# Performance work log

Hardware: AMD Instinct MI355X
Metric: run time of the kernel (lower is better)

The kernel has to match this reference:

```python
import jax, jax.numpy as jnp
import numpy as np

H, D, H1, L = 4, 128, 512, 2
EPS = 1e-5


def _seg_softmax(logits, seg, n):
    # numerically stable softmax over edges grouped by destination node
    mx = jax.ops.segment_max(logits, seg, num_segments=n)
    mx = jnp.where(jnp.isfinite(mx), mx, 0.0)
    e = jnp.exp(logits - mx[seg])
    s = jax.ops.segment_sum(e, seg, num_segments=n)
    return e / (s[seg] + 1e-16)


def _layernorm(x, g, b):
    mu = x.mean(-1, keepdims=True)
    var = ((x - mu) ** 2).mean(-1, keepdims=True)
    return (x - mu) * jax.lax.rsqrt(var + EPS) * g + b


def _hgt_forward(x_paper, x_author, Wp_paper, bp_paper, Wp_author, bp_author,
                 Wk, bk, Wq, bq, Wv, bv, Wa, ba, skip,
                 a_rel, m_rel, p_rel, ln_g, ln_b,
                 W256, b256, W128, b128,
                 ei_cites, ei_writes, ei_writtenby):
    Np, Na = x_paper.shape[0], x_author.shape[0]
    hp = x_paper @ Wp_paper + bp_paper   # [Np, 512]
    ha = x_author @ Wp_author + bp_author  # [Na, 512]
    scale = 1.0 / jnp.sqrt(jnp.float32(D))

    def kqv(h, l, t):
        k = (h @ Wk[l, t] + bk[l, t]).reshape(-1, H, D)
        q = (h @ Wq[l, t] + bq[l, t]).reshape(-1, H, D)
        v = (h @ Wv[l, t] + bv[l, t]).reshape(-1, H, D)
        return k, q, v

    def rel_msgs(k_src, v_src, q_dst, ei, l, r):
        src, dst = ei[0], ei[1]
        kr = jnp.einsum('nhd,hde->nhe', k_src, a_rel[l, r])  # per-src-node relation transform
        vr = jnp.einsum('nhd,hde->nhe', v_src, m_rel[l, r])
        alpha = (q_dst[dst] * kr[src]).sum(-1) * p_rel[l, r] * scale  # [E, H]
        return alpha, vr[src], dst

    for l in range(L):
        kp, qp, vp = kqv(hp, l, 0)
        ka, qa, va = kqv(ha, l, 1)
        # paper receives: cites (paper->paper, rel 0) + writes (author->paper, rel 1)
        a0, m0, d0 = rel_msgs(kp, vp, qp, ei_cites, l, 0)
        a1, m1, d1 = rel_msgs(ka, va, qp, ei_writes, l, 1)
        al = jnp.concatenate([a0, a1], 0)
        mg = jnp.concatenate([m0, m1], 0)
        ds = jnp.concatenate([d0, d1], 0)
        al = _seg_softmax(al, ds, Np)
        op = jax.ops.segment_sum(al[:, :, None] * mg, ds, num_segments=Np).reshape(Np, H1)
        # author receives: written_by (paper->author, rel 2)
        a2, m2, d2 = rel_msgs(kp, vp, qa, ei_writtenby, l, 2)
        a2 = _seg_softmax(a2, d2, Na)
        oa = jax.ops.segment_sum(a2[:, :, None] * m2, d2, num_segments=Na).reshape(Na, H1)
        # per-dst-type output linear on gelu, then sigmoid-gated skip (HGTConv)
        op = jax.nn.gelu(op, approximate=False) @ Wa[l, 0] + ba[l, 0]
        oa = jax.nn.gelu(oa, approximate=False) @ Wa[l, 1] + ba[l, 1]
        sp = jax.nn.sigmoid(skip[l, 0])
        sa = jax.nn.sigmoid(skip[l, 1])
        op = sp * op + (1.0 - sp) * hp
        oa = sa * oa + (1.0 - sa) * ha
        # encoder wrapper: residual + shared LayerNorm + ReLU (dropout = identity in eval)
        hp = jax.nn.relu(_layernorm(op + hp, ln_g[l], ln_b[l]))
        ha = jax.nn.relu(_layernorm(oa + ha, ln_g[l], ln_b[l]))

    hp = jax.nn.relu(hp @ W256 + b256) @ W128 + b128
    ha = jax.nn.relu(ha @ W256 + b256) @ W128 + b128
    return hp, ha


def setup_inputs() -> dict:
    key = jax.random.key(0)
    ks = iter(jax.random.split(key, 48))
    Np, Na, IN = 30000, 10000, 768
    Ec, Ew, Eb = 150000, 80000, 80000
    f = lambda *s: jax.random.normal(next(ks), s, jnp.float32) * 0.02
    ri = lambda n, e: jax.random.randint(next(ks), (e,), 0, n, jnp.int32)
    inp = {
        'x_paper': jax.random.normal(next(ks), (Np, IN), jnp.float32),
        'x_author': jax.random.normal(next(ks), (Na, IN), jnp.float32),
        'Wp_paper': f(IN, H1), 'bp_paper': jnp.zeros((H1,), jnp.float32),
        'Wp_author': f(IN, H1), 'bp_author': jnp.zeros((H1,), jnp.float32),
        'Wk': f(L, 2, H1, H1), 'bk': jnp.zeros((L, 2, H1), jnp.float32),
        'Wq': f(L, 2, H1, H1), 'bq': jnp.zeros((L, 2, H1), jnp.float32),
        'Wv': f(L, 2, H1, H1), 'bv': jnp.zeros((L, 2, H1), jnp.float32),
        'Wa': f(L, 2, H1, H1), 'ba': jnp.zeros((L, 2, H1), jnp.float32),
        'skip': jnp.ones((L, 2), jnp.float32),
        'a_rel': f(L, 3, H, D, D), 'm_rel': f(L, 3, H, D, D),
        'p_rel': jnp.ones((L, 3, H), jnp.float32),
        'ln_g': jnp.ones((L, H1), jnp.float32), 'ln_b': jnp.zeros((L, H1), jnp.float32),
        'W256': f(H1, 256), 'b256': jnp.zeros((256,), jnp.float32),
        'W128': f(256, 128), 'b128': jnp.zeros((128,), jnp.float32),
        'ei_cites': jnp.stack([ri(Np, Ec), ri(Np, Ec)]),
        'ei_writes': jnp.stack([ri(Na, Ew), ri(Np, Ew)]),
        'ei_writtenby': jnp.stack([ri(Np, Eb), ri(Na, Eb)]),
    }
    return inp


def reference(x_paper, x_author, Wp_paper, bp_paper, Wp_author, bp_author,
              Wk, bk, Wq, bq, Wv, bv, Wa, ba, skip,
              a_rel, m_rel, p_rel, ln_g, ln_b,
              W256, b256, W128, b128,
              ei_cites, ei_writes, ei_writtenby):
    return _hgt_forward(x_paper, x_author, Wp_paper, bp_paper, Wp_author, bp_author,
                        Wk, bk, Wq, bq, Wv, bv, Wa, ba, skip,
                        a_rel, m_rel, p_rel, ln_g, ln_b,
                        W256, b256, W128, b128,
                        ei_cites, ei_writes, ei_writtenby)
```

## Files before the change

kernel.cpp:

```cpp
#include <hip/hip_runtime.h>
#include <hip/hip_bf16.h>
#include <math.h>

#define NHEAD 4
#define DH 128
#define HID 512
#define NLAY 2
#define NP 30000
#define NA 10000
#define INDIM 768
#define EC 150000
#define EW 80000
#define EB 80000
#define NQP 2560
#define NQA 1536

typedef __hip_bfloat16 bf16;
typedef __attribute__((ext_vector_type(8))) short bf16x8;
typedef __attribute__((ext_vector_type(4))) float f32x4;
typedef __attribute__((ext_vector_type(4))) unsigned int u32x4;

__device__ __forceinline__ unsigned short f2bu(float f){ bf16 t = __float2bfloat16(f); return *(unsigned short*)&t; }
__device__ __forceinline__ float bu2f(unsigned short u){ return __uint_as_float((unsigned)u << 16); }

__device__ __forceinline__ void load8b(const bf16* __restrict__ p, int i8, float* o){
  uint4 r = ((const uint4*)p)[i8];
  o[0]=__uint_as_float(r.x<<16); o[1]=__uint_as_float(r.x&0xffff0000u);
  o[2]=__uint_as_float(r.y<<16); o[3]=__uint_as_float(r.y&0xffff0000u);
  o[4]=__uint_as_float(r.z<<16); o[5]=__uint_as_float(r.z&0xffff0000u);
  o[6]=__uint_as_float(r.w<<16); o[7]=__uint_as_float(r.w&0xffff0000u);
}

__device__ __forceinline__ void gload16(const void* g, void* l) {
  __builtin_amdgcn_global_load_lds((const __attribute__((address_space(1))) void*)g,
                                   (__attribute__((address_space(3))) void*)l, 16, 0, 0);
}

struct GemmPair {
  const bf16 *A0, *A1, *B0, *B1;
  const float *b0, *b1;
  void *C0, *C1;
  int lda0, lda1, ldb0, ldb1, ldc0, ldc1;
  int M0, M1, K0, K1;
  int act0, act1, bf0, bf1;
  int nbn0, nbn1, nw0;
};

#define TSTRIDE 132

__global__ __launch_bounds__(256)
void mfma_gemm2(GemmPair gp)
{
  __shared__ __align__(16) short smem[32768];
  const int tid = threadIdx.x;
  const int lane = tid & 63, w = tid >> 6;
  const int nwg = gridDim.x;
  const int bid = blockIdx.x;
  const int xcd = bid & 7, pos = bid >> 3;
  const int q8 = nwg >> 3, r8 = nwg & 7;
  const int work = (xcd < r8 ? xcd * (q8 + 1) : r8 * (q8 + 1) + (xcd - r8) * q8) + pos;
  const int g = work >= gp.nw0;
  const int w2 = g ? work - gp.nw0 : work;
  const bf16* A  = g ? gp.A1 : gp.A0;
  const bf16* Bt = g ? gp.B1 : gp.B0;
  const float* bias = g ? gp.b1 : gp.b0;
  void* Cv = g ? gp.C1 : gp.C0;
  const int lda = g ? gp.lda1 : gp.lda0;
  const int ldb = g ? gp.ldb1 : gp.ldb0;
  const int ldc = g ? gp.ldc1 : gp.ldc0;
  const int M = g ? gp.M1 : gp.M0;
  const int K = g ? gp.K1 : gp.K0;
  const int act = g ? gp.act1 : gp.act0;
  const int isbf = g ? gp.bf1 : gp.bf0;
  const int nbn = g ? gp.nbn1 : gp.nbn0;
  const int brow = (w2 / nbn) * 128, bcol = (w2 % nbn) * 128;
  const int wr = w >> 1, wc = w & 1;

  f32x4 acc[4][4];
#pragma unroll
  for (int m = 0; m < 4; m++)
#pragma unroll
    for (int n = 0; n < 4; n++) acc[m][n] = (f32x4){0.f, 0.f, 0.f, 0.f};

  auto STAGE = [&](int buf, int k0) {
    short* Asb = smem + buf * 8192;
    short* Bsb = smem + 16384 + buf * 8192;
#pragma unroll
    for (int i = 0; i < 4; i++) {
      int chunk = i * 4 + w;
      int c_lin = chunk * 64 + lane;
      int row = c_lin >> 3;
      int kc = ((c_lin & 7) ^ (row & 7)) * 8;
      int growA = brow + row; growA = growA < M ? growA : M - 1;
      gload16(A + (size_t)growA * lda + k0 + kc, Asb + chunk * 512);
      gload16(Bt + (size_t)(bcol + row) * ldb + k0 + kc, Bsb + chunk * 512);
    }
  };

  const int nk = K >> 6;
  STAGE(0, 0);
  __syncthreads();
  int buf = 0;
  for (int t = 0; t < nk; t++) {
    if (t + 1 < nk) STAGE(buf ^ 1, (t + 1) << 6);
    const short* Asb = smem + buf * 8192;
    const short* Bsb = smem + 16384 + buf * 8192;
#pragma unroll
    for (int kk = 0; kk < 2; kk++) {
      const int ke = kk * 32 + (lane >> 4) * 8;
      bf16x8 af[4], bq[4];
#pragma unroll
      for (int m = 0; m < 4; m++) {
        int row = wr * 64 + m * 16 + (lane & 15);
        af[m] = *(const bf16x8*)(Asb + row * 64 + (ke ^ ((row & 7) << 3)));
      }
#pragma unroll
      for (int n = 0; n < 4; n++) {
        int col = wc * 64 + n * 16 + (lane & 15);
        bq[n] = *(const bf16x8*)(Bsb + col * 64 + (ke ^ ((col & 7) << 3)));
      }
#pragma unroll
      for (int m = 0; m < 4; m++)
#pragma unroll
        for (int n = 0; n < 4; n++)
          acc[m][n] = __builtin_amdgcn_mfma_f32_16x16x32_bf16(af[m], bq[n], acc[m][n], 0, 0, 0);
    }
    __syncthreads();
    buf ^= 1;
  }

  if (isbf) {
#pragma unroll
    for (int m = 0; m < 4; m++) {
      int row0 = wr * 64 + m * 16 + (lane >> 4) * 4;
#pragma unroll
      for (int n = 0; n < 4; n++) {
        int col = wc * 64 + n * 16 + (lane & 15);
        float bv = bias ? bias[bcol + col] : 0.f;
#pragma unroll
        for (int r = 0; r < 4; r++) {
          float v = acc[m][n][r] + bv;
          if (act) v = fmaxf(v, 0.f);
          smem[(row0 + r) * TSTRIDE + col] = (short)f2bu(v);
        }
      }
    }
    __syncthreads();
#pragma unroll
    for (int it = 0; it < 8; it++) {
      int chunk = it * 256 + tid;
      int row = chunk >> 4, c16 = chunk & 15;
      int gr = brow + row;
      if (gr < M) {
        u32x4 v = *(const u32x4*)(smem + row * TSTRIDE + c16 * 8);
        __builtin_nontemporal_store(v,
            (u32x4*)((unsigned short*)Cv + (size_t)gr * ldc + bcol + c16 * 8));
      }
    }
  } else {
#pragma unroll
    for (int m = 0; m < 4; m++) {
      int gr0 = brow + wr * 64 + m * 16 + (lane >> 4) * 4;
#pragma unroll
      for (int n = 0; n < 4; n++) {
        int gc = bcol + wc * 64 + n * 16 + (lane & 15);
        float bv = bias ? bias[gc] : 0.f;
#pragma unroll
        for (int r = 0; r < 4; r++) {
          int gr = gr0 + r;
          if (gr < M) {
            float v = acc[m][n][r] + bv;
            if (act) v = fmaxf(v, 0.f);
            __builtin_nontemporal_store(v, (float*)Cv + (size_t)gr * ldc + gc);
          }
        }
      }
    }
  }
}

struct FuseArgs {
  const float* W[12];
  const float* rel[12];
  const float* bin[12];
  float* out[12];
  float* bout[12];
};
struct TrArgs {
  const float* src[20];
  bf16* dst[20];
};
struct CopyB { const float* src[4]; float* dst[4]; };

__global__ __launch_bounds__(256)
void gemm_fuse(FuseArgs fa)
{
  int c = blockIdx.z >> 2, h = blockIdx.z & 3;
  const float* A = fa.W[c] + h * 128;
  const float* B = fa.rel[c] + (size_t)h * 128 * 128;
  float* C = fa.out[c] + h * 128;
  __shared__ float Ast[64][17];
  __shared__ float Bst[16][64];
  const int tid = threadIdx.x;
  const int tx = tid & 15, ty = tid >> 4;
  const int bm = blockIdx.x * 64, bn = blockIdx.y * 64;
  float acc[4][4] = {};
  for (int k0 = 0; k0 < 128; k0 += 16) {
#pragma unroll
    for (int i = 0; i < 4; i++) {
      int lin = tid + i * 256;
      int m = lin >> 4, kk = lin & 15;
      Ast[m][kk] = A[(size_t)(bm + m) * 512 + k0 + kk];
      int kb = lin >> 6, nb = lin & 63;
      Bst[kb][nb] = B[(size_t)(k0 + kb) * 128 + bn + nb];
    }
    __syncthreads();
#pragma unroll
    for (int kk = 0; kk < 16; kk++) {
      float a[4], b[4];
#pragma unroll
      for (int i = 0; i < 4; i++) a[i] = Ast[ty * 4 + i][kk];
#pragma unroll
      for (int j = 0; j < 4; j++) b[j] = Bst[kk][tx * 4 + j];
#pragma unroll
      for (int i = 0; i < 4; i++)
#pragma unroll
        for (int j = 0; j < 4; j++)
          acc[i][j] = fmaf(a[i], b[j], acc[i][j]);
    }
    __syncthreads();
  }
#pragma unroll
  for (int i = 0; i < 4; i++)
#pragma unroll
    for (int j = 0; j < 4; j++)
      C[(size_t)(bm + ty * 4 + i) * 512 + bn + tx * 4 + j] = acc[i][j];
}

__global__ __launch_bounds__(256)
void transpose20(TrArgs ta)
{
  int c = blockIdx.z;
  const float* in = ta.src[c];
  bf16* o = ta.dst[c];
  __shared__ float t[32][33];
  int bn = blockIdx.x * 32, bk = blockIdx.y * 32;
  int x = threadIdx.x, y = threadIdx.y;
#pragma unroll
  for (int i = 0; i < 32; i += 8)
    t[y + i][x] = in[(size_t)(bk + y + i) * 512 + bn + x];
  __syncthreads();
#pragma unroll
  for (int i = 0; i < 32; i += 8)
    o[(size_t)(bn + y + i) * 512 + bk + x] = __float2bfloat16(t[x][y + i]);
}

__global__ __launch_bounds__(512)
void bias_fuse_all(FuseArgs fa)
{
  int c = blockIdx.x;
  int j = threadIdx.x;
  int h = j >> 7, e = j & 127;
  const float* bh = fa.bin[c] + h * DH;
  const float* rh = fa.rel[c] + (size_t)h * DH * DH;
  float s = 0.f;
  for (int d = 0; d < DH; d++) s = fmaf(bh[d], rh[d * DH + e], s);
  fa.bout[c][j] = s;
}

__global__ __launch_bounds__(512)
void copy_bias(CopyB cb)
{
  cb.dst[blockIdx.x][threadIdx.x] = cb.src[blockIdx.x][threadIdx.x];
}

__global__ __launch_bounds__(256)
void transpose_to_bf16(const float* __restrict__ in, bf16* __restrict__ out,
                       int K_, int N_)
{
  __shared__ float t[32][33];
  int bn = blockIdx.x * 32, bk = blockIdx.y * 32;
  int x = threadIdx.x, y = threadIdx.y;
#pragma unroll
  for (int i = 0; i < 32; i += 8) {
    int k = bk + y + i, n = bn + x;
    if (k < K_ && n < N_) t[y + i][x] = in[(size_t)k * N_ + n];
  }
  __syncthreads();
#pragma unroll
  for (int i = 0; i < 32; i += 8) {
    int n = bn + y + i, k = bk + x;
    if (n < N_ && k < K_) out[(size_t)n * K_ + k] = __float2bfloat16(t[x][y + i]);
  }
}

__global__ __launch_bounds__(256)
void f32_to_bf16_2(const float* __restrict__ s0, bf16* __restrict__ d0, long long n0,
                   const float* __restrict__ s1, bf16* __restrict__ d1, long long n1)
{
  long long i = ((long long)blockIdx.x * 256 + threadIdx.x) * 4;
  const float* s; bf16* d;
  if (i < n0) { s = s0; d = d0; }
  else { i -= n0; if (i >= n1) return; s = s1; d = d1; }
  float4 v = *(const float4*)(s + i);
  ushort4 o;
  o.x = f2bu(v.x); o.y = f2bu(v.y); o.z = f2bu(v.z); o.w = f2bu(v.w);
  *(ushort4*)(d + i) = o;
}

__global__ __launch_bounds__(256)
void build_hist(const int* __restrict__ ei_dst, int E, int* __restrict__ deg)
{
  int i = blockIdx.x * 256 + threadIdx.x;
  if (i < E) atomicAdd(&deg[ei_dst[i]], 1);
}

__global__ __launch_bounds__(256)
void scan_blk(const int* __restrict__ deg, int n, int* __restrict__ rowptr,
              int* __restrict__ bsum)
{
  __shared__ int sh[256];
  int t = threadIdx.x;
  int base = blockIdx.x * 1024 + t * 4;
  int v0 = 0, v1 = 0, v2 = 0, v3 = 0;
  if (base + 3 < n) {
    int4 v = *(const int4*)(deg + base);
    v0 = v.x; v1 = v.y; v2 = v.z; v3 = v.w;
  } else {
    if (base < n)     v0 = deg[base];
    if (base + 1 < n) v1 = deg[base + 1];
    if (base + 2 < n) v2 = deg[base + 2];
    if (base + 3 < n) v3 = deg[base + 3];
  }
  int s = v0 + v1 + v2 + v3;
  sh[t] = s;
  __syncthreads();
#pragma unroll
  for (int off = 1; off < 256; off <<= 1) {
    int tv = (t >= off) ? sh[t - off] : 0;
    __syncthreads();
    sh[t] += tv;
    __syncthreads();
  }
  int excl = sh[t] - s;
  if (t == 255) bsum[blockIdx.x] = sh[255];
  if (base < n)     rowptr[base] = excl;
  if (base + 1 < n) rowptr[base + 1] = excl + v0;
  if (base + 2 < n) rowptr[base + 2] = excl + v0 + v1;
  if (base + 3 < n) rowptr[base + 3] = excl + v0 + v1 + v2;
}

__global__ __launch_bounds__(64)
void scan_bsum(int* __restrict__ bsum, int nb, int* __restrict__ rowptr_end)
{
  int t = threadIdx.x;
  int v = (t < nb) ? bsum[t] : 0;
  int inc = v;
#pragma unroll
  for (int off = 1; off < 64; off <<= 1) {
    int o = __shfl_up(inc, off);
    if (t >= off) inc += o;
  }
  if (t < nb) bsum[t] = inc - v;
  if (t == nb - 1) *rowptr_end = inc;
}

__global__ __launch_bounds__(256)
void scan_add(int* __restrict__ rowptr, const int* __restrict__ bsum, int n)
{
  int add = bsum[blockIdx.x];
  if (add == 0) return;
  int i = blockIdx.x * 1024 + threadIdx.x * 4;
  if (i < n)     rowptr[i] += add;
  if (i + 1 < n) rowptr[i + 1] += add;
  if (i + 2 < n) rowptr[i + 2] += add;
  if (i + 3 < n) rowptr[i + 3] += add;
}

__global__ __launch_bounds__(256)
void build_scatter(const int* __restrict__ ei, int E, int flag,
                   const int* __restrict__ rowptr, int* __restrict__ cursor,
                   int* __restrict__ srcs)
{
  int e = blockIdx.x * 256 + threadIdx.x;
  if (e >= E) return;
  int src = ei[e];
  int dst = ei[E + e];
  int pos = rowptr[dst] + atomicAdd(&cursor[dst], 1);
  srcs[pos] = src | flag;
}

__global__ __launch_bounds__(256)
void csr_attn_agg2(const int* __restrict__ rowptrP, const int* __restrict__ srcsP,
                   const int* __restrict__ rowptrA, const int* __restrict__ srcsA,
                   const bf16* __restrict__ qkvP, const bf16* __restrict__ qkvA,
                   const float* __restrict__ prl, float scale,
                   bf16* __restrict__ agP, bf16* __restrict__ agA)
{
  int node = blockIdx.x * 4 + (threadIdx.x >> 6);
  int lane = threadIdx.x & 63;
  int h = lane >> 4;
  const int* rp; const int* srcs;
  const bf16* q; const bf16 *t0, *t1;
  int ld0, off0, ld1, off1;
  float p0, p1;
  bf16* outp;
  if (node < NP) {
    rp = rowptrP; srcs = srcsP;
    q = qkvP + (size_t)node * NQP;
    t0 = qkvP; ld0 = NQP; off0 = 512;
    t1 = qkvA; ld1 = NQA; off1 = 512;
    p0 = prl[h] * scale; p1 = prl[4 + h] * scale;
    outp = agP + (size_t)node * HID;
  } else {
    int r = node - NP;
    if (r >= NA) return;
    rp = rowptrA; srcs = srcsA; node = r;
    q = qkvA + (size_t)r * NQA;
    t0 = qkvP; ld0 = NQP; off0 = 1536;
    t1 = qkvP; ld1 = NQP; off1 = 1536;
    p0 = prl[8 + h] * scale; p1 = p0;
    outp = agA + (size_t)r * HID;
  }
  float qv[8];
  load8b(q, lane, qv);
  int beg = rp[node], end = rp[node + 1];
  float m = -INFINITY, s = 0.f;
  float acc[8] = {};
  for (int p = beg; p < end; ++p) {
    int se = srcs[p];
    int src = se & 0x3FFFFFFF;
    bool f1 = (se & 0x40000000) != 0;
    const bf16* row = f1 ? (t1 + (size_t)src * ld1 + off1)
                         : (t0 + (size_t)src * ld0 + off0);
    float kv[8], vv[8];
    load8b(row, lane, kv);
    load8b(row + 512, lane, vv);
    float a = 0.f;
#pragma unroll
    for (int i = 0; i < 8; i++) a = fmaf(qv[i], kv[i], a);
    a += __shfl_xor(a, 1);
    a += __shfl_xor(a, 2);
    a += __shfl_xor(a, 4);
    a += __shfl_xor(a, 8);
    a *= f1 ? p1 : p0;
    if (a > m + 8.f) {
      float sc = __expf(m - a);
      s *= sc;
#pragma unroll
      for (int i = 0; i < 8; i++) acc[i] *= sc;
      m = a;
    }
    float wgt = __expf(a - m);
    s += wgt;
#pragma unroll
    for (int i = 0; i < 8; i++) acc[i] = fmaf(wgt, vv[i], acc[i]);
  }
  float inv = 1.f / (s + 1e-16f);
  unsigned short gg[8];
#pragma unroll
  for (int i = 0; i < 8; i++) {
    float v = acc[i] * inv;
    gg[i] = f2bu(0.5f * v * (1.f + erff(v * 0.70710678118654752f)));
  }
  uint4 o;
  o.x = gg[0] | ((unsigned)gg[1] << 16);
  o.y = gg[2] | ((unsigned)gg[3] << 16);
  o.z = gg[4] | ((unsigned)gg[5] << 16);
  o.w = gg[6] | ((unsigned)gg[7] << 16);
  *(uint4*)(outp + lane * 8) = o;
}

__global__ __launch_bounds__(256)
void skip_ln_relu2(const bf16* __restrict__ oplP, const bf16* __restrict__ oplA,
                   bf16* __restrict__ hP, bf16* __restrict__ hA,
                   const float* __restrict__ skip2,
                   const float* __restrict__ g, const float* __restrict__ b)
{
  int row = blockIdx.x;
  const bf16* orow; bf16* hrow; float sk;
  if (row < NP) {
    orow = oplP + (size_t)row * HID; hrow = hP + (size_t)row * HID; sk = skip2[0];
  } else {
    int r = row - NP;
    orow = oplA + (size_t)r * HID; hrow = hA + (size_t)r * HID; sk = skip2[1];
  }
  float sp = 1.f / (1.f + expf(-sk));
  int t = threadIdx.x;
  ushort2 ov = ((const ushort2*)orow)[t];
  ushort2 hv = ((ushort2*)hrow)[t];
  float t0 = sp * bu2f(ov.x) + (2.f - sp) * bu2f(hv.x);
  float t1 = sp * bu2f(ov.y) + (2.f - sp) * bu2f(hv.y);
  float s = t0 + t1, ss = t0 * t0 + t1 * t1;
#pragma unroll
  for (int off = 32; off; off >>= 1) {
    s += __shfl_down(s, off);
    ss += __shfl_down(ss, off);
  }
  __shared__ float sh[8];
  int wid = t >> 6, lane = t & 63;
  if (lane == 0) { sh[wid] = s; sh[4 + wid] = ss; }
  __syncthreads();
  if (t == 0) {
    float S = 0, SS = 0;
    for (int wv = 0; wv < 4; wv++) { S += sh[wv]; SS += sh[4 + wv]; }
    sh[0] = S; sh[4] = SS;
  }
  __syncthreads();
  float mu = sh[0] * (1.f / 512.f);
  float var = sh[4] * (1.f / 512.f) - mu * mu;
  float inv = rsqrtf(var + 1e-5f);
  float y0 = (t0 - mu) * inv * g[2 * t] + b[2 * t];
  float y1 = (t1 - mu) * inv * g[2 * t + 1] + b[2 * t + 1];
  ushort2 o;
  o.x = f2bu(fmaxf(y0, 0.f));
  o.y = f2bu(fmaxf(y1, 0.f));
  ((ushort2*)hrow)[t] = o;
}

static inline void mgemm2(GemmPair gp, int N0, int N1, hipStream_t s)
{
  gp.nbn0 = N0 / 128;
  gp.nbn1 = N1 / 128;
  int nw0 = ((gp.M0 + 127) / 128) * gp.nbn0;
  int nw1 = ((gp.M1 + 127) / 128) * gp.nbn1;
  gp.nw0 = nw0;
  mfma_gemm2<<<dim3(nw0 + nw1), 256, 0, s>>>(gp);
}

extern "C" void kernel_launch(void* const* d_in, const int* in_sizes, int n_in,
                              void* d_out, int out_size, void* d_ws, size_t ws_size,
                              hipStream_t stream)
{
  const float* x_paper  = (const float*)d_in[0];
  const float* x_author = (const float*)d_in[1];
  const float* Wp_paper = (const float*)d_in[2];
  const float* bp_paper = (const float*)d_in[3];
  const float* Wp_author= (const float*)d_in[4];
  const float* bp_author= (const float*)d_in[5];
  const float* Wk = (const float*)d_in[6];
  const float* bk = (const float*)d_in[7];
  const float* Wq = (const float*)d_in[8];
  const float* bq = (const float*)d_in[9];
  const float* Wv = (const float*)d_in[10];
  const float* bv = (const float*)d_in[11];
  const float* Wa = (const float*)d_in[12];
  const float* ba = (const float*)d_in[13];
  const float* skip = (const float*)d_in[14];
  const float* a_rel = (const float*)d_in[15];
  const float* m_rel = (const float*)d_in[16];
  const float* p_rel = (const float*)d_in[17];
  const float* ln_g = (const float*)d_in[18];
  const float* ln_b = (const float*)d_in[19];
  const float* W256 = (const float*)d_in[20];
  const float* b256 = (const float*)d_in[21];
  const float* W128 = (const float*)d_in[22];
  const float* b128 = (const float*)d_in[23];
  const int* ei_c = (const int*)d_in[24];
  const int* ei_w = (const int*)d_in[25];
  const int* ei_b = (const int*)d_in[26];
  float* out = (float*)d_out;

  const size_t NPe = (size_t)NP * HID, NAe = (size_t)NA * HID;
  const size_t HH = (size_t)HID * HID;
  char* w = (char*)d_ws;
  size_t off = 0;
  auto alloc = [&](size_t bytes) -> void* {
    void* p = (void*)(w + off);
    off += (bytes + 255) & ~(size_t)255;
    return p;
  };
  bf16* hb_p  = (bf16*)alloc(NPe * 2);
  bf16* hb_a  = (bf16*)alloc(NAe * 2);
  bf16* qkv_p = (bf16*)alloc((size_t)NP * NQP * 2);
  bf16* qkv_a = (bf16*)alloc((size_t)NA * NQA * 2);
  bf16* ag_p  = (bf16*)alloc(NPe * 2);
  bf16* ag_a  = (bf16*)alloc(NAe * 2);
  float* Wf32 = (float*)alloc(12 * HH * 4);
  bf16* WBtP  = (bf16*)alloc((size_t)2 * NQP * HID * 2);
  bf16* WBtA  = (bf16*)alloc((size_t)2 * NQA * HID * 2);
  float* pbP  = (float*)alloc((size_t)2 * NQP * 4);
  float* pbA  = (float*)alloc((size_t)2 * NQA * 4);
  bf16* WaT   = (bf16*)alloc(4 * HH * 2);
  bf16* W256T = (bf16*)alloc((size_t)HID * 256 * 2);
  bf16* W128T = (bf16*)alloc((size_t)256 * 128 * 2);
  bf16* WpTp  = (bf16*)alloc((size_t)INDIM * HID * 2);
  bf16* WpTa  = (bf16*)alloc((size_t)INDIM * HID * 2);
  int* rowptrP = (int*)alloc((size_t)(NP + 1) * 4);
  int* degP    = (int*)alloc((size_t)NP * 4);
  int* srcsP   = (int*)alloc((size_t)(EC + EW) * 4);
  int* rowptrA = (int*)alloc((size_t)(NA + 1) * 4);
  int* degA    = (int*)alloc((size_t)NA * 4);
  int* srcsA   = (int*)alloc((size_t)EB * 4);
  int* bsumP   = (int*)alloc(64 * 4);
  int* bsumA   = (int*)alloc(64 * 4);
  if (off > ws_size) return;

  const float scale = 0.08838834764831845f;
  const int nbP = (NP + 1023) / 1024, nbA = (NA + 1023) / 1024;

  (void)hipMemsetAsync(degP, 0, (size_t)NP * 4, stream);
  (void)hipMemsetAsync(degA, 0, (size_t)NA * 4, stream);
  build_hist<<<dim3((EC + 255) / 256), 256, 0, stream>>>(ei_c + EC, EC, degP);
  build_hist<<<dim3((EW + 255) / 256), 256, 0, stream>>>(ei_w + EW, EW, degP);
  build_hist<<<dim3((EB + 255) / 256), 256, 0, stream>>>(ei_b + EB, EB, degA);
  scan_blk<<<dim3(nbP), 256, 0, stream>>>(degP, NP, rowptrP, bsumP);
  scan_bsum<<<dim3(1), 64, 0, stream>>>(bsumP, nbP, rowptrP + NP);
  scan_add<<<dim3(nbP), 256, 0, stream>>>(rowptrP, bsumP, NP);
  scan_blk<<<dim3(nbA), 256, 0, stream>>>(degA, NA, rowptrA, bsumA);
  scan_bsum<<<dim3(1), 64, 0, stream>>>(bsumA, nbA, rowptrA + NA);
  scan_add<<<dim3(nbA), 256, 0, stream>>>(rowptrA, bsumA, NA);
  (void)hipMemsetAsync(degP, 0, (size_t)NP * 4, stream);
  (void)hipMemsetAsync(degA, 0, (size_t)NA * 4, stream);
  build_scatter<<<dim3((EC + 255) / 256), 256, 0, stream>>>(ei_c, EC, 0,
      rowptrP, degP, srcsP);
  build_scatter<<<dim3((EW + 255) / 256), 256, 0, stream>>>(ei_w, EW, 0x40000000,
      rowptrP, degP, srcsP);
  build_scatter<<<dim3((EB + 255) / 256), 256, 0, stream>>>(ei_b, EB, 0,
      rowptrA, degA, srcsA);

  FuseArgs fa;
  TrArgs ta;
  CopyB cb;
  for (int l = 0; l < NLAY; l++) {
    bf16* packP = WBtP + (size_t)l * NQP * HID;
    bf16* packA = WBtA + (size_t)l * NQA * HID;
    float* pbPl = pbP + (size_t)l * NQP;
    float* pbAl = pbA + (size_t)l * NQA;
    for (int r = 0; r < 3; r++)
      for (int s = 0; s < 2; s++) {
        int c = (l * 3 + r) * 2 + s;
        int t = (r == 1) ? 1 : 0;
        fa.W[c]   = (s == 0 ? Wk : Wv) + (size_t)(l * 2 + t) * HH;
        fa.rel[c] = (s == 0 ? a_rel : m_rel) + (size_t)(l * 3 + r) * NHEAD * DH * DH;
        fa.bin[c] = (s == 0 ? bk : bv) + (size_t)(l * 2 + t) * HID;
        fa.out[c] = Wf32 + (size_t)c * HH;
        ta.src[c] = fa.out[c];
        if (r == 0) {
          ta.dst[c]  = packP + (size_t)(512 + s * 512) * HID;
          fa.bout[c] = pbPl + 512 + s * 512;
        } else if (r == 1) {
          ta.dst[c]  = packA + (size_t)(512 + s * 512) * HID;
          fa.bout[c] = pbAl + 512 + s * 512;
        } else {
          ta.dst[c]  = packP + (size_t)(1536 + s * 512) * HID;
          fa.bout[c] = pbPl + 1536 + s * 512;
        }
      }
    ta.src[12 + l * 2 + 0] = Wq + (size_t)(l * 2 + 0) * HH;
    ta.dst[12 + l * 2 + 0] = packP;
    ta.src[12 + l * 2 + 1] = Wq + (size_t)(l * 2 + 1) * HH;
    ta.dst[12 + l * 2 + 1] = packA;
    ta.src[16 + l * 2 + 0] = Wa + (size_t)(l * 2 + 0) * HH;
    ta.dst[16 + l * 2 + 0] = WaT + (size_t)(l * 2 + 0) * HH;
    ta.src[16 + l * 2 + 1] = Wa + (size_t)(l * 2 + 1) * HH;
    ta.dst[16 + l * 2 + 1] = WaT + (size_t)(l * 2 + 1) * HH;
    cb.src[l * 2 + 0] = bq + (size_t)(l * 2 + 0) * HID;
    cb.dst[l * 2 + 0] = pbPl;
    cb.src[l * 2 + 1] = bq + (size_t)(l * 2 + 1) * HID;
    cb.dst[l * 2 + 1] = pbAl;
  }
  gemm_fuse<<<dim3(8, 2, 48), 256, 0, stream>>>(fa);
  transpose20<<<dim3(16, 16, 20), dim3(32, 8), 0, stream>>>(ta);
  bias_fuse_all<<<dim3(12), 512, 0, stream>>>(fa);
  copy_bias<<<dim3(4), 512, 0, stream>>>(cb);
  {
    dim3 b(32, 8);
    transpose_to_bf16<<<dim3(8, 16), b, 0, stream>>>(W256, W256T, HID, 256);
    transpose_to_bf16<<<dim3(4, 8), b, 0, stream>>>(W128, W128T, 256, 128);
    transpose_to_bf16<<<dim3(16, 24), b, 0, stream>>>(Wp_paper, WpTp, INDIM, HID);
    transpose_to_bf16<<<dim3(16, 24), b, 0, stream>>>(Wp_author, WpTa, INDIM, HID);
  }

  bf16* xb_p = qkv_p;
  bf16* xb_a = qkv_a;
  long long nxp = (long long)NP * INDIM, nxa = (long long)NA * INDIM;
  f32_to_bf16_2<<<dim3((int)(((nxp + nxa) / 4 + 255) / 256)), 256, 0, stream>>>(
      x_paper, xb_p, nxp, x_author, xb_a, nxa);
  {
    GemmPair gp{};
    gp.A0 = xb_p; gp.lda0 = INDIM; gp.B0 = WpTp; gp.ldb0 = INDIM;
    gp.b0 = bp_paper; gp.C0 = hb_p; gp.ldc0 = HID;
    gp.M0 = NP; gp.K0 = INDIM; gp.act0 = 0; gp.bf0 = 1;
    gp.A1 = xb_a; gp.lda1 = INDIM; gp.B1 = WpTa; gp.ldb1 = INDIM;
    gp.b1 = bp_author; gp.C1 = hb_a; gp.ldc1 = HID;
    gp.M1 = NA; gp.K1 = INDIM; gp.act1 = 0; gp.bf1 = 1;
    mgemm2(gp, HID, HID, stream);
  }

  for (int l = 0; l < NLAY; l++) {
    const float* prl = p_rel + (size_t)l * 3 * NHEAD;
    const bf16* packP = WBtP + (size_t)l * NQP * HID;
    const bf16* packA = WBtA + (size_t)l * NQA * HID;
    const float* pbPl = pbP + (size_t)l * NQP;
    const float* pbAl = pbA + (size_t)l * NQA;

    {
      GemmPair gp{};
      gp.A0 = hb_p; gp.lda0 = HID; gp.B0 = packP; gp.ldb0 = HID;
      gp.b0 = pbPl; gp.C0 = qkv_p; gp.ldc0 = NQP;
      gp.M0 = NP; gp.K0 = HID; gp.act0 = 0; gp.bf0 = 1;
      gp.A1 = hb_a; gp.lda1 = HID; gp.B1 = packA; gp.ldb1 = HID;
      gp.b1 = pbAl; gp.C1 = qkv_a; gp.ldc1 = NQA;
      gp.M1 = NA; gp.K1 = HID; gp.act1 = 0; gp.bf1 = 1;
      mgemm2(gp, NQP, NQA, stream);
    }
    csr_attn_agg2<<<dim3((NP + NA + 3) / 4), 256, 0, stream>>>(
        rowptrP, srcsP, rowptrA, srcsA, qkv_p, qkv_a, prl, scale, ag_p, ag_a);
    bf16* opl_p = qkv_p;
    bf16* opl_a = qkv_a;
    {
      GemmPair gp{};
      gp.A0 = ag_p; gp.lda0 = HID; gp.B0 = WaT + (size_t)(l * 2 + 0) * HH; gp.ldb0 = HID;
      gp.b0 = ba + (size_t)(l * 2 + 0) * HID; gp.C0 = opl_p; gp.ldc0 = HID;
      gp.M0 = NP; gp.K0 = HID; gp.act0 = 0; gp.bf0 = 1;
      gp.A1 = ag_a; gp.lda1 = HID; gp.B1 = WaT + (size_t)(l * 2 + 1) * HH; gp.ldb1 = HID;
      gp.b1 = ba + (size_t)(l * 2 + 1) * HID; gp.C1 = opl_a; gp.ldc1 = HID;
      gp.M1 = NA; gp.K1 = HID; gp.act1 = 0; gp.bf1 = 1;
      mgemm2(gp, HID, HID, stream);
    }
    skip_ln_relu2<<<dim3(NP + NA), 256, 0, stream>>>(
        opl_p, opl_a, hb_p, hb_a, skip + l * 2,
        ln_g + (size_t)l * HID, ln_b + (size_t)l * HID);
  }

  bf16* h256_p = ag_p;
  bf16* h256_a = ag_a;
  {
    GemmPair gp{};
    gp.A0 = hb_p; gp.lda0 = HID; gp.B0 = W256T; gp.ldb0 = HID;
    gp.b0 = b256; gp.C0 = h256_p; gp.ldc0 = 256;
    gp.M0 = NP; gp.K0 = HID; gp.act0 = 1; gp.bf0 = 1;
    gp.A1 = hb_a; gp.lda1 = HID; gp.B1 = W256T; gp.ldb1 = HID;
    gp.b1 = b256; gp.C1 = h256_a; gp.ldc1 = 256;
    gp.M1 = NA; gp.K1 = HID; gp.act1 = 1; gp.bf1 = 1;
    mgemm2(gp, 256, 256, stream);
  }
  {
    GemmPair gp{};
    gp.A0 = h256_p; gp.lda0 = 256; gp.B0 = W128T; gp.ldb0 = 256;
    gp.b0 = b128; gp.C0 = out; gp.ldc0 = 128;
    gp.M0 = NP; gp.K0 = 256; gp.act0 = 0; gp.bf0 = 0;
    gp.A1 = h256_a; gp.lda1 = 256; gp.B1 = W128T; gp.ldb1 = 256;
    gp.b1 = b128; gp.C1 = out + (size_t)NP * 128; gp.ldc1 = 128;
    gp.M1 = NA; gp.K1 = 256; gp.act1 = 0; gp.bf1 = 0;
    mgemm2(gp, 128, 128, stream);
  }
}
```

Before: 898.1 us.

## Merge CSR build launches and single-buffer GEMM shared memory

The per-relation histogram, scan and scatter kernels are merged into combined launches covering all three edge sets, with a single memset for degree and cursor arrays. This cuts roughly a dozen launches and memsets down to six. Separately, the GEMM drops its double-buffered LDS pipeline for a single buffer sized for the epilogue transpose, loading and syncing before each k-step. That lowers LDS use and may allow more resident blocks, but global loads no longer overlap MFMA work.

```diff
diff --git a/kernel.cpp b/kernel.cpp
--- a/kernel.cpp
+++ b/kernel.cpp
@@ -51,7 +51,7 @@
 __global__ __launch_bounds__(256)
 void mfma_gemm2(GemmPair gp)
 {
-  __shared__ __align__(16) short smem[32768];
+  __shared__ __align__(16) short smem[128 * TSTRIDE];
   const int tid = threadIdx.x;
   const int lane = tid & 63, w = tid >> 6;
   const int nwg = gridDim.x;
@@ -82,9 +82,11 @@
 #pragma unroll
     for (int n = 0; n < 4; n++) acc[m][n] = (f32x4){0.f, 0.f, 0.f, 0.f};
 
-  auto STAGE = [&](int buf, int k0) {
-    short* Asb = smem + buf * 8192;
-    short* Bsb = smem + 16384 + buf * 8192;
+  short* Asb = smem;
+  short* Bsb = smem + 8192;
+  const int nk = K >> 6;
+  for (int t = 0; t < nk; t++) {
+    const int k0 = t << 6;
 #pragma unroll
     for (int i = 0; i < 4; i++) {
       int chunk = i * 4 + w;
@@ -95,16 +97,7 @@
       gload16(A + (size_t)growA * lda + k0 + kc, Asb + chunk * 512);
       gload16(Bt + (size_t)(bcol + row) * ldb + k0 + kc, Bsb + chunk * 512);
     }
-  };
-
-  const int nk = K >> 6;
-  STAGE(0, 0);
-  __syncthreads();
-  int buf = 0;
-  for (int t = 0; t < nk; t++) {
-    if (t + 1 < nk) STAGE(buf ^ 1, (t + 1) << 6);
-    const short* Asb = smem + buf * 8192;
-    const short* Bsb = smem + 16384 + buf * 8192;
+    __syncthreads();
 #pragma unroll
     for (int kk = 0; kk < 2; kk++) {
       const int ke = kk * 32 + (lane >> 4) * 8;
@@ -126,7 +119,6 @@
           acc[m][n] = __builtin_amdgcn_mfma_f32_16x16x32_bf16(af[m], bq[n], acc[m][n], 0, 0, 0);
     }
     __syncthreads();
-    buf ^= 1;
   }
 
   if (isbf) {
@@ -309,19 +301,23 @@
 }
 
 __global__ __launch_bounds__(256)
-void build_hist(const int* __restrict__ ei_dst, int E, int* __restrict__ deg)
+void build_hist3(const int* __restrict__ eiC, const int* __restrict__ eiW,
+                 const int* __restrict__ eiB,
+                 int* __restrict__ degP, int* __restrict__ degA)
 {
   int i = blockIdx.x * 256 + threadIdx.x;
-  if (i < E) atomicAdd(&deg[ei_dst[i]], 1);
-}
-
-__global__ __launch_bounds__(256)
-void scan_blk(const int* __restrict__ deg, int n, int* __restrict__ rowptr,
-              int* __restrict__ bsum)
+  if (i < EC) atomicAdd(&degP[eiC[EC + i]], 1);
+  else if (i < EC + EW) atomicAdd(&degP[eiW[EW + (i - EC)]], 1);
+  else if (i < EC + EW + EB) atomicAdd(&degA[eiB[EB + (i - EC - EW)]], 1);
+}
+
+__device__ __forceinline__ void scan_blk_body(const int* __restrict__ deg, int n,
+                                              int* __restrict__ rowptr,
+                                              int* __restrict__ bsum, int blk)
 {
   __shared__ int sh[256];
   int t = threadIdx.x;
-  int base = blockIdx.x * 1024 + t * 4;
+  int base = blk * 1024 + t * 4;
   int v0 = 0, v1 = 0, v2 = 0, v3 = 0;
   if (base + 3 < n) {
     int4 v = *(const int4*)(deg + base);
@@ -343,16 +339,31 @@
     __syncthreads();
   }
   int excl = sh[t] - s;
-  if (t == 255) bsum[blockIdx.x] = sh[255];
+  if (t == 255) bsum[blk] = sh[255];
   if (base < n)     rowptr[base] = excl;
   if (base + 1 < n) rowptr[base + 1] = excl + v0;
   if (base + 2 < n) rowptr[base + 2] = excl + v0 + v1;
   if (base + 3 < n) rowptr[base + 3] = excl + v0 + v1 + v2;
 }
 
+#define NBP ((NP + 1023) / 1024)
+#define NBA ((NA + 1023) / 1024)
+
+__global__ __launch_bounds__(256)
+void scan_blk2(const int* __restrict__ degP, int* __restrict__ rowptrP, int* __restrict__ bsumP,
+               const int* __restrict__ degA, int* __restrict__ rowptrA, int* __restrict__ bsumA)
+{
+  if (blockIdx.x < NBP) scan_blk_body(degP, NP, rowptrP, bsumP, blockIdx.x);
+  else                  scan_blk_body(degA, NA, rowptrA, bsumA, blockIdx.x - NBP);
+}
+
 __global__ __launch_bounds__(64)
-void scan_bsum(int* __restrict__ bsum, int nb, int* __restrict__ rowptr_end)
-{
+void scan_bsum2(int* __restrict__ bsumP, int* __restrict__ endP,
+                int* __restrict__ bsumA, int* __restrict__ endA)
+{
+  int* bsum = blockIdx.x ? bsumA : bsumP;
+  int nb = blockIdx.x ? NBA : NBP;
+  int* rpe = blockIdx.x ? endA : endP;
   int t = threadIdx.x;
   int v = (t < nb) ? bsum[t] : 0;
   int inc = v;
@@ -362,15 +373,19 @@
     if (t >= off) inc += o;
   }
   if (t < nb) bsum[t] = inc - v;
-  if (t == nb - 1) *rowptr_end = inc;
-}
-
-__global__ __launch_bounds__(256)
-void scan_add(int* __restrict__ rowptr, const int* __restrict__ bsum, int n)
-{
-  int add = bsum[blockIdx.x];
+  if (t == nb - 1) *rpe = inc;
+}
+
+__global__ __launch_bounds__(256)
+void scan_add2(int* __restrict__ rowptrP, const int* __restrict__ bsumP,
+               int* __restrict__ rowptrA, const int* __restrict__ bsumA)
+{
+  int* rowptr; const int* bsum; int n, blk;
+  if (blockIdx.x < NBP) { rowptr = rowptrP; bsum = bsumP; n = NP; blk = blockIdx.x; }
+  else                  { rowptr = rowptrA; bsum = bsumA; n = NA; blk = blockIdx.x - NBP; }
+  int add = bsum[blk];
   if (add == 0) return;
-  int i = blockIdx.x * 1024 + threadIdx.x * 4;
+  int i = blk * 1024 + threadIdx.x * 4;
   if (i < n)     rowptr[i] += add;
   if (i + 1 < n) rowptr[i + 1] += add;
   if (i + 2 < n) rowptr[i + 2] += add;
@@ -378,16 +393,29 @@
 }
 
 __global__ __launch_bounds__(256)
-void build_scatter(const int* __restrict__ ei, int E, int flag,
-                   const int* __restrict__ rowptr, int* __restrict__ cursor,
-                   int* __restrict__ srcs)
-{
-  int e = blockIdx.x * 256 + threadIdx.x;
-  if (e >= E) return;
-  int src = ei[e];
-  int dst = ei[E + e];
-  int pos = rowptr[dst] + atomicAdd(&cursor[dst], 1);
-  srcs[pos] = src | flag;
+void build_scatter3(const int* __restrict__ eiC, const int* __restrict__ eiW,
+                    const int* __restrict__ eiB,
+                    const int* __restrict__ rowptrP, int* __restrict__ curP,
+                    int* __restrict__ srcsP,
+                    const int* __restrict__ rowptrA, int* __restrict__ curA,
+                    int* __restrict__ srcsA)
+{
+  int i = blockIdx.x * 256 + threadIdx.x;
+  if (i < EC) {
+    int src = eiC[i], dst = eiC[EC + i];
+    int pos = rowptrP[dst] + atomicAdd(&curP[dst], 1);
+    srcsP[pos] = src;
+  } else if (i < EC + EW) {
+    int e = i - EC;
+    int src = eiW[e], dst = eiW[EW + e];
+    int pos = rowptrP[dst] + atomicAdd(&curP[dst], 1);
+    srcsP[pos] = src | 0x40000000;
+  } else if (i < EC + EW + EB) {
+    int e = i - EC - EW;
+    int src = eiB[e], dst = eiB[EB + e];
+    int pos = rowptrA[dst] + atomicAdd(&curA[dst], 1);
+    srcsA[pos] = src;
+  }
 }
 
 __global__ __launch_bounds__(256)
@@ -587,37 +615,26 @@
   bf16* WpTp  = (bf16*)alloc((size_t)INDIM * HID * 2);
   bf16* WpTa  = (bf16*)alloc((size_t)INDIM * HID * 2);
   int* rowptrP = (int*)alloc((size_t)(NP + 1) * 4);
-  int* degP    = (int*)alloc((size_t)NP * 4);
+  int* rowptrA = (int*)alloc((size_t)(NA + 1) * 4);
+  int* degP    = (int*)alloc((size_t)(2 * NP + 2 * NA) * 4);
+  int* degA    = degP + NP;
+  int* curP    = degA + NA;
+  int* curA    = curP + NP;
   int* srcsP   = (int*)alloc((size_t)(EC + EW) * 4);
-  int* rowptrA = (int*)alloc((size_t)(NA + 1) * 4);
-  int* degA    = (int*)alloc((size_t)NA * 4);
   int* srcsA   = (int*)alloc((size_t)EB * 4);
   int* bsumP   = (int*)alloc(64 * 4);
   int* bsumA   = (int*)alloc(64 * 4);
   if (off > ws_size) return;
 
   const float scale = 0.08838834764831845f;
-  const int nbP = (NP + 1023) / 1024, nbA = (NA + 1023) / 1024;
-
-  (void)hipMemsetAsync(degP, 0, (size_t)NP * 4, stream);
-  (void)hipMemsetAsync(degA, 0, (size_t)NA * 4, stream);
-  build_hist<<<dim3((EC + 255) / 256), 256, 0, stream>>>(ei_c + EC, EC, degP);
-  build_hist<<<dim3((EW + 255) / 256), 256, 0, stream>>>(ei_w + EW, EW, degP);
-  build_hist<<<dim3((EB + 255) / 256), 256, 0, stream>>>(ei_b + EB, EB, degA);
-  scan_blk<<<dim3(nbP), 256, 0, stream>>>(degP, NP, rowptrP, bsumP);
-  scan_bsum<<<dim3(1), 64, 0, stream>>>(bsumP, nbP, rowptrP + NP);
-  scan_add<<<dim3(nbP), 256, 0, stream>>>(rowptrP, bsumP, NP);
-  scan_blk<<<dim3(nbA), 256, 0, stream>>>(degA, NA, rowptrA, bsumA);
-  scan_bsum<<<dim3(1), 64, 0, stream>>>(bsumA, nbA, rowptrA + NA);
-  scan_add<<<dim3(nbA), 256, 0, stream>>>(rowptrA, bsumA, NA);
-  (void)hipMemsetAsync(degP, 0, (size_t)NP * 4, stream);
-  (void)hipMemsetAsync(degA, 0, (size_t)NA * 4, stream);
-  build_scatter<<<dim3((EC + 255) / 256), 256, 0, stream>>>(ei_c, EC, 0,
-      rowptrP, degP, srcsP);
-  build_scatter<<<dim3((EW + 255) / 256), 256, 0, stream>>>(ei_w, EW, 0x40000000,
-      rowptrP, degP, srcsP);
-  build_scatter<<<dim3((EB + 255) / 256), 256, 0, stream>>>(ei_b, EB, 0,
-      rowptrA, degA, srcsA);
+
+  (void)hipMemsetAsync(degP, 0, (size_t)(2 * NP + 2 * NA) * 4, stream);
+  build_hist3<<<dim3((EC + EW + EB + 255) / 256), 256, 0, stream>>>(ei_c, ei_w, ei_b, degP, degA);
+  scan_blk2<<<dim3(NBP + NBA), 256, 0, stream>>>(degP, rowptrP, bsumP, degA, rowptrA, bsumA);
+  scan_bsum2<<<dim3(2), 64, 0, stream>>>(bsumP, rowptrP + NP, bsumA, rowptrA + NA);
+  scan_add2<<<dim3(NBP + NBA), 256, 0, stream>>>(rowptrP, bsumP, rowptrA, bsumA);
+  build_scatter3<<<dim3((EC + EW + EB + 255) / 256), 256, 0, stream>>>(
+      ei_c, ei_w, ei_b, rowptrP, curP, srcsP, rowptrA, curA, srcsA);
 
   FuseArgs fa;
   TrArgs ta;
```

Result: faster. 844.1 us (-6.0%).
